# Optimization experiments

Measured on AMD Instinct MI355X. Metric: run time of the kernel, lower is better.

## Reference

```python
import jax, jax.numpy as jnp
import numpy as np

N = 8192
F_IN = 128
F_OUT = 64
NEG_INF = -9e15


def setup_inputs() -> dict:
    key = jax.random.key(0)
    k1, k2, k3, k4 = jax.random.split(key, 4)
    x = jax.random.normal(k1, (N, F_IN), dtype=jnp.float32)
    adj = jax.random.randint(k2, (N, N), 0, 2, dtype=jnp.int32)
    W = jax.random.normal(k3, (F_OUT, F_IN), dtype=jnp.float32) * 0.05  # torch Linear weight [out,in]
    a = jax.random.normal(k4, (1, 2 * F_OUT), dtype=jnp.float32) * 0.05  # attention vector weight [1, 2*out]
    return {"x": x, "adj": adj, "W": W, "a": a}


def reference(x, adj, W, a):
    fout = W.shape[0]
    Wh = x @ W.T                                   # [N, out]
    a1 = a[0, :fout]                               # a.weight.T[:out]
    a2 = a[0, fout:]                               # a.weight.T[out:]
    Wh1 = Wh @ a1                                  # [N]
    Wh2 = Wh @ a2                                  # [N]
    e = jax.nn.leaky_relu(Wh1[:, None] + Wh2[None, :], negative_slope=0.2)  # [N, N]
    attention = jnp.where(adj > 0, e, NEG_INF)
    attention = jax.nn.softmax(attention, axis=1)
    # dropout is identity in eval / deterministic reference
    h_prime = attention @ Wh                       # [N, out]
    return jax.nn.elu(h_prime)
```

## Files before the change

kernel.cpp:

```cpp
#include <hip/hip_runtime.h>
#include <cstdint>
#include <cstddef>

#define NN 8192
#define FIN 128
#define FOUT 64

typedef __attribute__((ext_vector_type(8))) short short8;
typedef __attribute__((ext_vector_type(4))) float f32x4;

__device__ __forceinline__ unsigned short f32_to_bf16_bits(float f) {
    union { float f; uint32_t u; } c; c.f = f;
    uint32_t u = c.u;
    u += 0x7fffu + ((u >> 16) & 1u);
    return (unsigned short)(u >> 16);
}

__device__ __forceinline__ unsigned int pack_bf16(float lo, float hi) {
    return (unsigned int)f32_to_bf16_bits(lo) |
           ((unsigned int)f32_to_bf16_bits(hi) << 16);
}

__global__ __launch_bounds__(256) void gat_prep(
    const float* __restrict__ x, const float* __restrict__ W,
    const float* __restrict__ a, unsigned short* __restrict__ WhT,
    float* __restrict__ Wh1, float* __restrict__ Wh2)
{
    const int t    = threadIdx.x;
    const int f    = t & 63;
    const int iloc = t >> 6;
    const int i    = blockIdx.x * 4 + iloc;

    const float4* x4 = (const float4*)(x + (size_t)i * FIN);
    const float4* w4 = (const float4*)(W + (size_t)f * FIN);

    float acc = 0.f;
#pragma unroll
    for (int k = 0; k < FIN / 4; ++k) {
        float4 xv = x4[k];
        float4 wv = w4[k];
        acc += xv.x * wv.x + xv.y * wv.y + xv.z * wv.z + xv.w * wv.w;
    }

    WhT[(size_t)f * NN + i] = f32_to_bf16_bits(acc);

    float r1 = acc * a[f];
    float r2 = acc * a[64 + f];
#pragma unroll
    for (int m = 1; m < 64; m <<= 1) {
        r1 += __shfl_xor(r1, m, 64);
        r2 += __shfl_xor(r2, m, 64);
    }
    if (f == 0) { Wh1[i] = r1; Wh2[i] = r2; }
}

__global__ __launch_bounds__(256) void gat_attn(
    const int* __restrict__ adj, const unsigned short* __restrict__ WhT,
    const float* __restrict__ Wh1, const float* __restrict__ Wh2,
    float* __restrict__ out)
{
    __shared__ float lds_C[4][16][64];
    __shared__ float lds_tot[4][16];

    const int tid  = threadIdx.x;
    const int wave = tid >> 6;
    const int lane = tid & 63;
    const int il   = lane & 15;
    const int q    = lane >> 4;
    const int i0   = blockIdx.x * 16;
    const int i    = i0 + il;

    const float wh1    = Wh1[i];
    const int   jbase  = wave * 32 + q * 8;
    const int* __restrict__ adjrow = adj + (size_t)i * NN;

    const short8* bp0 = (const short8*)(WhT + (size_t)(0  + il) * NN);
    const short8* bp1 = (const short8*)(WhT + (size_t)(16 + il) * NN);
    const short8* bp2 = (const short8*)(WhT + (size_t)(32 + il) * NN);
    const short8* bp3 = (const short8*)(WhT + (size_t)(48 + il) * NN);

    f32x4 acc0 = {0.f, 0.f, 0.f, 0.f};
    f32x4 acc1 = {0.f, 0.f, 0.f, 0.f};
    f32x4 acc2 = {0.f, 0.f, 0.f, 0.f};
    f32x4 acc3 = {0.f, 0.f, 0.f, 0.f};
    float tot = 0.f;

    for (int tt = 0; tt < 64; ++tt) {
        const int j = tt * 128 + jbase;

        const int4   av0 = *(const int4*)(adjrow + j);
        const int4   av1 = *(const int4*)(adjrow + j + 4);
        const float4 w20 = *(const float4*)(Wh2 + j);
        const float4 w21 = *(const float4*)(Wh2 + j + 4);

        float wv[8];
#define CALC(idx, adjv, wh2v)                                          \
        {                                                              \
            float s = wh1 + (wh2v);                                    \
            float e = fmaxf(s, 0.2f * s);          \
            float v = ((adjv) > 0) ? __expf(e) : 0.f;                  \
            tot += v;                                                  \
            wv[idx] = v;                                               \
        }
        CALC(0, av0.x, w20.x) CALC(1, av0.y, w20.y)
        CALC(2, av0.z, w20.z) CALC(3, av0.w, w20.w)
        CALC(4, av1.x, w21.x) CALC(5, av1.y, w21.y)
        CALC(6, av1.z, w21.z) CALC(7, av1.w, w21.w)
#undef CALC

        union { short8 v; unsigned int u[4]; } af;
        af.u[0] = pack_bf16(wv[0], wv[1]);
        af.u[1] = pack_bf16(wv[2], wv[3]);
        af.u[2] = pack_bf16(wv[4], wv[5]);
        af.u[3] = pack_bf16(wv[6], wv[7]);

        const int jb = j >> 3;
        const short8 b0 = bp0[jb];
        const short8 b1 = bp1[jb];
        const short8 b2 = bp2[jb];
        const short8 b3 = bp3[jb];

        acc0 = __builtin_amdgcn_mfma_f32_16x16x32_bf16(af.v, b0, acc0, 0, 0, 0);
        acc1 = __builtin_amdgcn_mfma_f32_16x16x32_bf16(af.v, b1, acc1, 0, 0, 0);
        acc2 = __builtin_amdgcn_mfma_f32_16x16x32_bf16(af.v, b2, acc2, 0, 0, 0);
        acc3 = __builtin_amdgcn_mfma_f32_16x16x32_bf16(af.v, b3, acc3, 0, 0, 0);
    }

    tot += __shfl_xor(tot, 16, 64);
    tot += __shfl_xor(tot, 32, 64);
    if (lane < 16) lds_tot[wave][lane] = tot;

#pragma unroll
    for (int r = 0; r < 4; ++r) {
        lds_C[wave][q * 4 + r][0 * 16 + il] = acc0[r];
        lds_C[wave][q * 4 + r][1 * 16 + il] = acc1[r];
        lds_C[wave][q * 4 + r][2 * 16 + il] = acc2[r];
        lds_C[wave][q * 4 + r][3 * 16 + il] = acc3[r];
    }
    __syncthreads();

#pragma unroll
    for (int e = 0; e < 4; ++e) {
        const int idx = e * 256 + tid;
        const int ii = idx >> 6;
        const int ff = idx & 63;
        float s = lds_C[0][ii][ff] + lds_C[1][ii][ff] +
                  lds_C[2][ii][ff] + lds_C[3][ii][ff];
        float ts = lds_tot[0][ii] + lds_tot[1][ii] +
                   lds_tot[2][ii] + lds_tot[3][ii];
        float p = s / ts;
        out[(size_t)(i0 + ii) * FOUT + ff] = (p > 0.f) ? p : (__expf(p) - 1.f);
    }
}

extern "C" void kernel_launch(void* const* d_in, const int* in_sizes, int n_in,
                              void* d_out, int out_size, void* d_ws, size_t ws_size,
                              hipStream_t stream) {
    const float* x   = (const float*)d_in[0];
    const int*   adj = (const int*)d_in[1];
    const float* W   = (const float*)d_in[2];
    const float* a   = (const float*)d_in[3];
    float* out = (float*)d_out;

    unsigned short* WhT = (unsigned short*)d_ws;
    float* Wh1 = (float*)((char*)d_ws + (size_t)1048576);
    float* Wh2 = (float*)((char*)d_ws + (size_t)1048576 + 32768);

    gat_prep<<<dim3(NN / 4), dim3(256), 0, stream>>>(x, W, a, WhT, Wh1, Wh2);
    gat_attn<<<dim3(NN / 16), dim3(256), 0, stream>>>(adj, WhT, Wh1, Wh2, out);
}
```

Measured before the change: 432.4 us.

## Split attention columns across two blocks, prefetch next tile, add combine kernel

Splits each 16-row tile's column range into two halves handled by separate blocks, which doubles the grid to 1024 blocks. Partial numerators and softmax denominators go to workspace and are merged by a new combine kernel that applies the division and ELU. The main loop also software-prefetches the next iteration's adjacency, Wh2 and WhT loads into registers, adds launch bounds for 4 blocks per SM, and pads the LDS rows. In exchange it adds a third launch, writes and reads about 4MB of partials, and raises register pressure from the prefetch.

```diff
diff --git a/kernel.cpp b/kernel.cpp
--- a/kernel.cpp
+++ b/kernel.cpp
@@ -54,12 +54,12 @@
     if (f == 0) { Wh1[i] = r1; Wh2[i] = r2; }
 }
 
-__global__ __launch_bounds__(256) void gat_attn(
+__global__ __launch_bounds__(256, 4) void gat_attn(
     const int* __restrict__ adj, const unsigned short* __restrict__ WhT,
     const float* __restrict__ Wh1, const float* __restrict__ Wh2,
-    float* __restrict__ out)
+    float* __restrict__ Cpart, float* __restrict__ Tpart)
 {
-    __shared__ float lds_C[4][16][64];
+    __shared__ float lds_C[4][16][68];
     __shared__ float lds_tot[4][16];
 
     const int tid  = threadIdx.x;
@@ -67,11 +67,13 @@
     const int lane = tid & 63;
     const int il   = lane & 15;
     const int q    = lane >> 4;
-    const int i0   = blockIdx.x * 16;
+    const int rt   = blockIdx.x >> 1;
+    const int jh   = blockIdx.x & 1;
+    const int i0   = rt * 16;
     const int i    = i0 + il;
 
-    const float wh1    = Wh1[i];
-    const int   jbase  = wave * 32 + q * 8;
+    const float wh1   = Wh1[i];
+    const int   jbase = jh * 4096 + wave * 32 + q * 8;
     const int* __restrict__ adjrow = adj + (size_t)i * NN;
 
     const short8* bp0 = (const short8*)(WhT + (size_t)(0  + il) * NN);
@@ -85,13 +87,27 @@
     f32x4 acc3 = {0.f, 0.f, 0.f, 0.f};
     float tot = 0.f;
 
-    for (int tt = 0; tt < 64; ++tt) {
-        const int j = tt * 128 + jbase;
-
-        const int4   av0 = *(const int4*)(adjrow + j);
-        const int4   av1 = *(const int4*)(adjrow + j + 4);
-        const float4 w20 = *(const float4*)(Wh2 + j);
-        const float4 w21 = *(const float4*)(Wh2 + j + 4);
+    int4   av0 = *(const int4*)(adjrow + jbase);
+    int4   av1 = *(const int4*)(adjrow + jbase + 4);
+    float4 w20 = *(const float4*)(Wh2 + jbase);
+    float4 w21 = *(const float4*)(Wh2 + jbase + 4);
+    int jb = jbase >> 3;
+    short8 b0 = bp0[jb];
+    short8 b1 = bp1[jb];
+    short8 b2 = bp2[jb];
+    short8 b3 = bp3[jb];
+
+    for (int tt = 0; tt < 32; ++tt) {
+        const int jn = jbase + (((tt + 1) & 31) << 7);
+        const int4   nav0 = *(const int4*)(adjrow + jn);
+        const int4   nav1 = *(const int4*)(adjrow + jn + 4);
+        const float4 nw20 = *(const float4*)(Wh2 + jn);
+        const float4 nw21 = *(const float4*)(Wh2 + jn + 4);
+        const int jnb = jn >> 3;
+        const short8 nb0 = bp0[jnb];
+        const short8 nb1 = bp1[jnb];
+        const short8 nb2 = bp2[jnb];
+        const short8 nb3 = bp3[jnb];
 
         float wv[8];
 #define CALC(idx, adjv, wh2v)                                          \
@@ -114,16 +130,13 @@
         af.u[2] = pack_bf16(wv[4], wv[5]);
         af.u[3] = pack_bf16(wv[6], wv[7]);
 
-        const int jb = j >> 3;
-        const short8 b0 = bp0[jb];
-        const short8 b1 = bp1[jb];
-        const short8 b2 = bp2[jb];
-        const short8 b3 = bp3[jb];
-
         acc0 = __builtin_amdgcn_mfma_f32_16x16x32_bf16(af.v, b0, acc0, 0, 0, 0);
         acc1 = __builtin_amdgcn_mfma_f32_16x16x32_bf16(af.v, b1, acc1, 0, 0, 0);
         acc2 = __builtin_amdgcn_mfma_f32_16x16x32_bf16(af.v, b2, acc2, 0, 0, 0);
         acc3 = __builtin_amdgcn_mfma_f32_16x16x32_bf16(af.v, b3, acc3, 0, 0, 0);
+
+        av0 = nav0; av1 = nav1; w20 = nw20; w21 = nw21;
+        b0 = nb0; b1 = nb1; b2 = nb2; b3 = nb3;
     }
 
     tot += __shfl_xor(tot, 16, 64);
@@ -146,11 +159,25 @@
         const int ff = idx & 63;
         float s = lds_C[0][ii][ff] + lds_C[1][ii][ff] +
                   lds_C[2][ii][ff] + lds_C[3][ii][ff];
-        float ts = lds_tot[0][ii] + lds_tot[1][ii] +
-                   lds_tot[2][ii] + lds_tot[3][ii];
-        float p = s / ts;
-        out[(size_t)(i0 + ii) * FOUT + ff] = (p > 0.f) ? p : (__expf(p) - 1.f);
-    }
+        Cpart[((size_t)jh * NN + i0 + ii) * FOUT + ff] = s;
+        if (ff == 0) {
+            float ts = lds_tot[0][ii] + lds_tot[1][ii] +
+                       lds_tot[2][ii] + lds_tot[3][ii];
+            Tpart[(size_t)jh * NN + i0 + ii] = ts;
+        }
+    }
+}
+
+__global__ __launch_bounds__(256) void gat_combine(
+    const float* __restrict__ Cpart, const float* __restrict__ Tpart,
+    float* __restrict__ out)
+{
+    const int idx = blockIdx.x * 256 + threadIdx.x;
+    const int i = idx >> 6;
+    const float c = Cpart[idx] + Cpart[(size_t)NN * FOUT + idx];
+    const float t = Tpart[i] + Tpart[NN + i];
+    const float p = c / t;
+    out[idx] = (p > 0.f) ? p : (__expf(p) - 1.f);
 }
 
 extern "C" void kernel_launch(void* const* d_in, const int* in_sizes, int n_in,
@@ -162,10 +189,14 @@
     const float* a   = (const float*)d_in[3];
     float* out = (float*)d_out;
 
-    unsigned short* WhT = (unsigned short*)d_ws;
-    float* Wh1 = (float*)((char*)d_ws + (size_t)1048576);
-    float* Wh2 = (float*)((char*)d_ws + (size_t)1048576 + 32768);
+    char* ws = (char*)d_ws;
+    unsigned short* WhT = (unsigned short*)ws;
+    float* Wh1   = (float*)(ws + (size_t)1048576);
+    float* Wh2   = (float*)(ws + (size_t)1048576 + 32768);
+    float* Cpart = (float*)(ws + (size_t)2097152);
+    float* Tpart = (float*)(ws + (size_t)6291456);
 
     gat_prep<<<dim3(NN / 4), dim3(256), 0, stream>>>(x, W, a, WhT, Wh1, Wh2);
-    gat_attn<<<dim3(NN / 16), dim3(256), 0, stream>>>(adj, WhT, Wh1, Wh2, out);
-}
+    gat_attn<<<dim3(NN / 16 * 2), dim3(256), 0, stream>>>(adj, WhT, Wh1, Wh2, Cpart, Tpart);
+    gat_combine<<<dim3(NN * FOUT / 256), dim3(256), 0, stream>>>(Cpart, Tpart, out);
+}
```

After: 423.4 us. -2.1%, faster.

## Stage adjacency through LDS as byte masks with coalesced double-buffered prefetch

Applied to the files above, without the earlier changes.

The attention kernel now loads adjacency rows with fully coalesced int4 reads, compresses each value to a byte mask, and stores them in a double-buffered, skewed LDS buffer that all waves read back to gate the exponentials. The next 1024-column chunk is prefetched into registers while the current one is processed, and the block grows to 8 waves with launch bounds for 4 blocks per CU. This targets the strided per-lane adjacency reads of the previous layout, which is the dominant HBM stream. In exchange it adds a barrier per chunk, more LDS traffic and register pressure, and a padded final reduction across 8 waves.

```diff
diff --git a/kernel.cpp b/kernel.cpp
--- a/kernel.cpp
+++ b/kernel.cpp
@@ -54,13 +54,15 @@
     if (f == 0) { Wh1[i] = r1; Wh2[i] = r2; }
 }
 
-__global__ __launch_bounds__(256) void gat_attn(
+__global__ __launch_bounds__(512, 4) void gat_attn(
     const int* __restrict__ adj, const unsigned short* __restrict__ WhT,
     const float* __restrict__ Wh1, const float* __restrict__ Wh2,
     float* __restrict__ out)
 {
-    __shared__ float lds_C[4][16][64];
-    __shared__ float lds_tot[4][16];
+    __shared__ __align__(16) unsigned char smem[35328];
+    unsigned char* maskbuf = smem;
+    float* ldsC = (float*)smem;
+    float* ldsT = (float*)(smem + 34816);
 
     const int tid  = threadIdx.x;
     const int wave = tid >> 6;
@@ -70,9 +72,12 @@
     const int i0   = blockIdx.x * 16;
     const int i    = i0 + il;
 
-    const float wh1    = Wh1[i];
-    const int   jbase  = wave * 32 + q * 8;
-    const int* __restrict__ adjrow = adj + (size_t)i * NN;
+    const float wh1 = Wh1[i];
+
+    const int r0     = wave * 2 + (lane >> 5);
+    const int cchunk = lane & 31;
+    const int4* __restrict__ arow =
+        (const int4*)(adj + (size_t)(i0 + r0) * NN) + cchunk;
 
     const short8* bp0 = (const short8*)(WhT + (size_t)(0  + il) * NN);
     const short8* bp1 = (const short8*)(WhT + (size_t)(16 + il) * NN);
@@ -85,70 +90,109 @@
     f32x4 acc3 = {0.f, 0.f, 0.f, 0.f};
     float tot = 0.f;
 
-    for (int tt = 0; tt < 64; ++tt) {
-        const int j = tt * 128 + jbase;
-
-        const int4   av0 = *(const int4*)(adjrow + j);
-        const int4   av1 = *(const int4*)(adjrow + j + 4);
-        const float4 w20 = *(const float4*)(Wh2 + j);
-        const float4 w21 = *(const float4*)(Wh2 + j + 4);
-
-        float wv[8];
-#define CALC(idx, adjv, wh2v)                                          \
-        {                                                              \
-            float s = wh1 + (wh2v);                                    \
-            float e = fmaxf(s, 0.2f * s);          \
-            float v = ((adjv) > 0) ? __expf(e) : 0.f;                  \
-            tot += v;                                                  \
-            wv[idx] = v;                                               \
-        }
-        CALC(0, av0.x, w20.x) CALC(1, av0.y, w20.y)
-        CALC(2, av0.z, w20.z) CALC(3, av0.w, w20.w)
-        CALC(4, av1.x, w21.x) CALC(5, av1.y, w21.y)
-        CALC(6, av1.z, w21.z) CALC(7, av1.w, w21.w)
+    int4 pre[8];
+
+#pragma unroll
+    for (int k = 0; k < 8; ++k) pre[k] = arow[k * 32];
+#pragma unroll
+    for (int k = 0; k < 8; ++k) {
+        const int4 v = pre[k];
+        const unsigned m = ((unsigned)v.x & 1u) | (((unsigned)v.y & 1u) << 8) |
+                           (((unsigned)v.z & 1u) << 16) | (((unsigned)v.w & 1u) << 24);
+        const int c4 = (cchunk + 32 * k) * 4;
+        *(unsigned*)(maskbuf + r0 * 1024 + ((c4 + r0 * 8) & 1023)) = m;
+    }
+    __syncthreads();
+
+    for (int s = 0; s < 8; ++s) {
+        if (s < 7) {
+#pragma unroll
+            for (int k = 0; k < 8; ++k) pre[k] = arow[(s + 1) * 256 + k * 32];
+        }
+
+        const unsigned char* mbuf = maskbuf + (s & 1) * 16384;
+#pragma unroll
+        for (int u = 0; u < 4; ++u) {
+            const int c0 = (wave * 4 + u) * 32 + q * 8;
+            const int j  = s * 1024 + c0;
+
+            const uint2 mb = *(const uint2*)(mbuf + il * 1024 + ((c0 + il * 8) & 1023));
+            const float4 w20 = *(const float4*)(Wh2 + j);
+            const float4 w21 = *(const float4*)(Wh2 + j + 4);
+
+            float wv[8];
+#define CALC(idx, mword, bit, wh2v)                                    \
+            {                                                          \
+                float sx = wh1 + (wh2v);                               \
+                float e = fmaxf(sx, 0.2f * sx);        \
+                float v = ((mword >> (bit)) & 1u) ? __expf(e) : 0.f;   \
+                tot += v;                                              \
+                wv[idx] = v;                                           \
+            }
+            CALC(0, mb.x, 0,  w20.x) CALC(1, mb.x, 8,  w20.y)
+            CALC(2, mb.x, 16, w20.z) CALC(3, mb.x, 24, w20.w)
+            CALC(4, mb.y, 0,  w21.x) CALC(5, mb.y, 8,  w21.y)
+            CALC(6, mb.y, 16, w21.z) CALC(7, mb.y, 24, w21.w)
 #undef CALC
 
-        union { short8 v; unsigned int u[4]; } af;
-        af.u[0] = pack_bf16(wv[0], wv[1]);
-        af.u[1] = pack_bf16(wv[2], wv[3]);
-        af.u[2] = pack_bf16(wv[4], wv[5]);
-        af.u[3] = pack_bf16(wv[6], wv[7]);
-
-        const int jb = j >> 3;
-        const short8 b0 = bp0[jb];
-        const short8 b1 = bp1[jb];
-        const short8 b2 = bp2[jb];
-        const short8 b3 = bp3[jb];
-
-        acc0 = __builtin_amdgcn_mfma_f32_16x16x32_bf16(af.v, b0, acc0, 0, 0, 0);
-        acc1 = __builtin_amdgcn_mfma_f32_16x16x32_bf16(af.v, b1, acc1, 0, 0, 0);
-        acc2 = __builtin_amdgcn_mfma_f32_16x16x32_bf16(af.v, b2, acc2, 0, 0, 0);
-        acc3 = __builtin_amdgcn_mfma_f32_16x16x32_bf16(af.v, b3, acc3, 0, 0, 0);
+            union { short8 v; unsigned int u4[4]; } af;
+            af.u4[0] = pack_bf16(wv[0], wv[1]);
+            af.u4[1] = pack_bf16(wv[2], wv[3]);
+            af.u4[2] = pack_bf16(wv[4], wv[5]);
+            af.u4[3] = pack_bf16(wv[6], wv[7]);
+
+            const int jb = j >> 3;
+            const short8 b0 = bp0[jb];
+            const short8 b1 = bp1[jb];
+            const short8 b2 = bp2[jb];
+            const short8 b3 = bp3[jb];
+
+            acc0 = __builtin_amdgcn_mfma_f32_16x16x32_bf16(af.v, b0, acc0, 0, 0, 0);
+            acc1 = __builtin_amdgcn_mfma_f32_16x16x32_bf16(af.v, b1, acc1, 0, 0, 0);
+            acc2 = __builtin_amdgcn_mfma_f32_16x16x32_bf16(af.v, b2, acc2, 0, 0, 0);
+            acc3 = __builtin_amdgcn_mfma_f32_16x16x32_bf16(af.v, b3, acc3, 0, 0, 0);
+        }
+
+        if (s < 7) {
+            unsigned char* wb = maskbuf + ((s + 1) & 1) * 16384;
+#pragma unroll
+            for (int k = 0; k < 8; ++k) {
+                const int4 v = pre[k];
+                const unsigned m = ((unsigned)v.x & 1u) | (((unsigned)v.y & 1u) << 8) |
+                                   (((unsigned)v.z & 1u) << 16) | (((unsigned)v.w & 1u) << 24);
+                const int c4 = (cchunk + 32 * k) * 4;
+                *(unsigned*)(wb + r0 * 1024 + ((c4 + r0 * 8) & 1023)) = m;
+            }
+        }
+        __syncthreads();
     }
 
     tot += __shfl_xor(tot, 16, 64);
     tot += __shfl_xor(tot, 32, 64);
-    if (lane < 16) lds_tot[wave][lane] = tot;
+    if (lane < 16) ldsT[wave * 16 + lane] = tot;
 
 #pragma unroll
     for (int r = 0; r < 4; ++r) {
-        lds_C[wave][q * 4 + r][0 * 16 + il] = acc0[r];
-        lds_C[wave][q * 4 + r][1 * 16 + il] = acc1[r];
-        lds_C[wave][q * 4 + r][2 * 16 + il] = acc2[r];
-        lds_C[wave][q * 4 + r][3 * 16 + il] = acc3[r];
+        float* row = ldsC + ((size_t)wave * 16 + (q * 4 + r)) * 68;
+        row[0 * 16 + il] = acc0[r];
+        row[1 * 16 + il] = acc1[r];
+        row[2 * 16 + il] = acc2[r];
+        row[3 * 16 + il] = acc3[r];
     }
     __syncthreads();
 
 #pragma unroll
-    for (int e = 0; e < 4; ++e) {
-        const int idx = e * 256 + tid;
+    for (int e = 0; e < 2; ++e) {
+        const int idx = e * 512 + tid;
         const int ii = idx >> 6;
         const int ff = idx & 63;
-        float s = lds_C[0][ii][ff] + lds_C[1][ii][ff] +
-                  lds_C[2][ii][ff] + lds_C[3][ii][ff];
-        float ts = lds_tot[0][ii] + lds_tot[1][ii] +
-                   lds_tot[2][ii] + lds_tot[3][ii];
-        float p = s / ts;
+        float sC = 0.f, sT = 0.f;
+#pragma unroll
+        for (int w = 0; w < 8; ++w) {
+            sC += ldsC[((size_t)w * 16 + ii) * 68 + ff];
+            sT += ldsT[w * 16 + ii];
+        }
+        const float p = sC / sT;
         out[(size_t)(i0 + ii) * FOUT + ff] = (p > 0.f) ? p : (__expf(p) - 1.f);
     }
 }
@@ -162,10 +206,11 @@
     const float* a   = (const float*)d_in[3];
     float* out = (float*)d_out;
 
-    unsigned short* WhT = (unsigned short*)d_ws;
-    float* Wh1 = (float*)((char*)d_ws + (size_t)1048576);
-    float* Wh2 = (float*)((char*)d_ws + (size_t)1048576 + 32768);
+    char* ws = (char*)d_ws;
+    unsigned short* WhT = (unsigned short*)ws;
+    float* Wh1 = (float*)(ws + (size_t)1048576);
+    float* Wh2 = (float*)(ws + (size_t)1048576 + 32768);
 
     gat_prep<<<dim3(NN / 4), dim3(256), 0, stream>>>(x, W, a, WhT, Wh1, Wh2);
-    gat_attn<<<dim3(NN / 16), dim3(256), 0, stream>>>(adj, WhT, Wh1, Wh2, out);
-}
+    gat_attn<<<dim3(NN / 16), dim3(512), 0, stream>>>(adj, WhT, Wh1, Wh2, out);
+}
```

After: 433.2 us. No clear change (+0.2%).
